# Optimization experiments

Hardware: AMD Instinct MI355X
Metric: run time of the kernel (lower is better)

## Reference

```python
import jax, jax.numpy as jnp
import numpy as np

GRID_SIZE = 5
SPLINE_ORDER = 3
NUM_BASIS = GRID_SIZE + SPLINE_ORDER  # 8
GRID = jnp.linspace(-1.0, 1.0, GRID_SIZE + 2 * SPLINE_ORDER + 1)  # [12]
EPS = 1e-6


def bspline_basis(x):
    """Iterative Cox-de Boor. x: [...]; returns [..., NUM_BASIS]."""
    xe = x[..., None]
    # order-0 indicator basis: [..., G-1]
    B = ((xe >= GRID[:-1]) & (xe < GRID[1:])).astype(x.dtype)
    for k in range(1, SPLINE_ORDER + 1):
        nb = B.shape[-1] - 1
        g_i = GRID[:nb]
        g_i1 = GRID[1:1 + nb]
        g_ik = GRID[k:k + nb]
        g_ik1 = GRID[k + 1:k + 1 + nb]
        dl = g_ik - g_i
        dr = g_ik1 - g_i1
        left = jnp.where(dl > EPS, (xe - g_i) / jnp.where(dl > EPS, dl, 1.0), 0.0) * B[..., :nb]
        right = jnp.where(dr > EPS, (g_ik1 - xe) / jnp.where(dr > EPS, dr, 1.0), 0.0) * B[..., 1:nb + 1]
        B = left + right
    return B[..., :NUM_BASIS]


def setup_inputs() -> dict:
    key = jax.random.key(0)
    k1, k2 = jax.random.split(key)
    x = jax.random.normal(k1, (8192, 512), dtype=jnp.float32)
    spline_coeffs = jax.random.normal(k2, (512, 512, NUM_BASIS), dtype=jnp.float32) * 0.1
    return {"x": x, "spline_coeffs": spline_coeffs}


def reference(x, spline_coeffs):
    xn = jnp.tanh(x)                       # [B, in]
    basis = bspline_basis(xn)              # [B, in, K]
    # output[b, o] = sum_{i,k} coeffs[o, i, k] * basis[b, i, k]
    return jnp.einsum('bik,oik->bo', basis, spline_coeffs)
```

## Files before the change

### kernel.cpp

```cpp
#include <hip/hip_runtime.h>
#include <hip/hip_bf16.h>
#include <stdint.h>


#define M_TOTAL 8192
#define N_DIM   512
#define K_DIM   4096
#define BM 128
#define BN 128
#define BK 64
#define NT_HALF 32
#define GRP_LDS 65536
#define BUF_HALF 32768

typedef __attribute__((ext_vector_type(8))) short short8;
typedef __attribute__((ext_vector_type(4))) float f32x4;
typedef __attribute__((ext_vector_type(16))) float f32x16;

typedef const __attribute__((address_space(1))) uint32_t ga_u32;
typedef __attribute__((address_space(3))) uint32_t ls_u32;

__device__ __forceinline__ void gload_lds16(const void* g, void* l) {
  __builtin_amdgcn_global_load_lds((ga_u32*)(uintptr_t)g,
                                   (ls_u32*)(uint32_t)(uintptr_t)l, 16, 0, 0);
}

__device__ __forceinline__ uint32_t f2bf(float f) {
  uint32_t u = __builtin_bit_cast(uint32_t, f);
  return (u + 0x7FFFu + ((u >> 16) & 1u)) >> 16;
}

__device__ __forceinline__ int swz(int r, int c) {
  return c ^ (r & 7) ^ (((r >> 4) & 1) << 2);
}

__device__ __forceinline__ void basis_slots(float xv, uint32_t o[4]) {
  xv = fminf(15.f, fmaxf(-15.f, xv));
  float e  = __expf(2.0f * xv);
  float t  = (e - 1.0f) * __builtin_amdgcn_rcpf(e + 1.0f);
  float uf = (t + 1.0f) * 5.5f;
  int   c  = (int)uf;  c = c > 10 ? 10 : c;
  float u  = uf - (float)c;
  float u2 = u * u, u3 = u2 * u, om = 1.0f - u;
  float w0 = om * om * om * (1.0f / 6.0f);
  float w1 = (3.0f * u3 - 6.0f * u2 + 4.0f) * (1.0f / 6.0f);
  float w2 = (-3.0f * u3 + 3.0f * u2 + 3.0f * u + 1.0f) * (1.0f / 6.0f);
  float w3 = u3 * (1.0f / 6.0f);
  uint32_t p01 = f2bf(w0) | (f2bf(w1) << 16);
  uint32_t p23 = f2bf(w2) | (f2bf(w3) << 16);
  uint64_t W = (uint64_t)p01 | ((uint64_t)p23 << 32);
  int d = c - 3;
  uint64_t lo = (d < 0) ? (W >> ((-d) * 16))
              : ((d < 4) ? (W << (d * 16)) : 0ull);
  uint64_t hi = (d <= 0) ? 0ull
              : ((d < 4) ? (W >> ((4 - d) * 16)) : (W << ((d - 4) * 16)));
  o[0] = (uint32_t)lo; o[1] = (uint32_t)(lo >> 32);
  o[2] = (uint32_t)hi; o[3] = (uint32_t)(hi >> 32);
}

__global__ __launch_bounds__(256) void basis_kernel(const float* __restrict__ x,
                                                    __hip_bfloat16* __restrict__ A,
                                                    int total) {
  int idx = blockIdx.x * 256 + threadIdx.x;
  if (idx >= total) return;
  uint32_t o[4];
  basis_slots(x[idx], o);
  reinterpret_cast<int4*>(A)[idx] = make_int4(o[0], o[1], o[2], o[3]);
}

__global__ __launch_bounds__(256) void cvt_kernel(const float* __restrict__ c,
                                                  __hip_bfloat16* __restrict__ Bt,
                                                  int total8) {
  int idx = blockIdx.x * 256 + threadIdx.x;
  if (idx >= total8) return;
  const float4* cp = reinterpret_cast<const float4*>(c) + (size_t)idx * 2;
  float4 a = cp[0], b = cp[1];
  union { unsigned short us[8]; int4 v; } pk;
  pk.us[0] = (unsigned short)f2bf(a.x); pk.us[1] = (unsigned short)f2bf(a.y);
  pk.us[2] = (unsigned short)f2bf(a.z); pk.us[3] = (unsigned short)f2bf(a.w);
  pk.us[4] = (unsigned short)f2bf(b.x); pk.us[5] = (unsigned short)f2bf(b.y);
  pk.us[6] = (unsigned short)f2bf(b.z); pk.us[7] = (unsigned short)f2bf(b.w);
  reinterpret_cast<int4*>(Bt)[idx] = pk.v;
}

__global__ __launch_bounds__(512) void gemm_kernel(
    const __hip_bfloat16* __restrict__ A,
    const __hip_bfloat16* __restrict__ Bt,
    float* __restrict__ C) {
  __shared__ char lds[2 * GRP_LDS];

  const int tid   = threadIdx.x;
  const int wid   = tid >> 6;
  const int lane  = tid & 63;
  const int l32   = lane & 31;
  const int lh    = lane >> 5;
  const int kgrp  = wid >> 2;
  const int w2    = wid & 3;
  const int waveM = w2 >> 1, waveN = w2 & 1;
  const int tg    = tid & 255;

  const int b  = blockIdx.x;
  const int q  = b >> 3;
  const int mt = (b & 7) * 8 + (q >> 2);
  const int nt = q & 3;
  const int m0 = mt * BM;
  const int n0 = nt * BN;

  char* grp = lds + kgrp * GRP_LDS;

  uint32_t aGlob[4], bGlob[4], sOff[4];
#pragma unroll
  for (int t = 0; t < 4; ++t) {
    int s = t * 256 + tg, row = s >> 3, p = s & 7, cc = swz(row, p);
    sOff[t]  = (uint32_t)s * 16u;
    aGlob[t] = (uint32_t)(m0 + row) * K_DIM + (uint32_t)cc * 8u
             + (uint32_t)kgrp * 2048u;
    bGlob[t] = (uint32_t)(n0 + row) * K_DIM + (uint32_t)cc * 8u
             + (uint32_t)kgrp * 2048u;
  }

  uint32_t aOff[4][2], bOff[4][2];
#pragma unroll
  for (int ks = 0; ks < 4; ++ks) {
    int c = ks * 2 + lh;
#pragma unroll
    for (int mi = 0; mi < 2; ++mi) {
      int row = waveM * 64 + mi * 32 + l32;
      aOff[ks][mi] = (uint32_t)(row * 8 + swz(row, c)) * 16u;
    }
#pragma unroll
    for (int ni = 0; ni < 2; ++ni) {
      int row = waveN * 64 + ni * 32 + l32;
      bOff[ks][ni] = 16384u + (uint32_t)(row * 8 + swz(row, c)) * 16u;
    }
  }

  f32x16 acc[2][2];
#pragma unroll
  for (int mi = 0; mi < 2; ++mi)
#pragma unroll
    for (int ni = 0; ni < 2; ++ni)
      acc[mi][ni] = (f32x16){0.f};

#pragma unroll
  for (int t = 0; t < 4; ++t) {
    gload_lds16(A + aGlob[t], grp + sOff[t]);
    gload_lds16(Bt + bGlob[t], grp + 16384 + sOff[t]);
  }

  for (int it = 0; it < NT_HALF; ++it) {
    const int cur = it & 1;
    char* bufc = grp + cur * BUF_HALF;
    __syncthreads();
    if (it + 1 < NT_HALF) {
      char* bufn = grp + (1 - cur) * BUF_HALF;
      uint32_t kt = (uint32_t)(it + 1) * BK;
#pragma unroll
      for (int t = 0; t < 4; ++t) {
        gload_lds16(A + aGlob[t] + kt, bufn + sOff[t]);
        gload_lds16(Bt + bGlob[t] + kt, bufn + 16384 + sOff[t]);
      }
    }
#pragma unroll
    for (int ks = 0; ks < 4; ++ks) {
      short8 af0 = *reinterpret_cast<const short8*>(bufc + aOff[ks][0]);
      short8 af1 = *reinterpret_cast<const short8*>(bufc + aOff[ks][1]);
      short8 bf0 = *reinterpret_cast<const short8*>(bufc + bOff[ks][0]);
      short8 bf1 = *reinterpret_cast<const short8*>(bufc + bOff[ks][1]);
      acc[0][0] = __builtin_amdgcn_mfma_f32_32x32x16_bf16(af0, bf0, acc[0][0], 0, 0, 0);
      acc[0][1] = __builtin_amdgcn_mfma_f32_32x32x16_bf16(af0, bf1, acc[0][1], 0, 0, 0);
      acc[1][0] = __builtin_amdgcn_mfma_f32_32x32x16_bf16(af1, bf0, acc[1][0], 0, 0, 0);
      acc[1][1] = __builtin_amdgcn_mfma_f32_32x32x16_bf16(af1, bf1, acc[1][1], 0, 0, 0);
    }
  }

  __syncthreads();
  if (kgrp == 1) {
#pragma unroll
    for (int mi = 0; mi < 2; ++mi)
#pragma unroll
      for (int ni = 0; ni < 2; ++ni) {
        int f = mi * 2 + ni;
#pragma unroll
        for (int j = 0; j < 4; ++j) {
          f32x4 v;
#pragma unroll
          for (int rr = 0; rr < 4; ++rr) v[rr] = acc[mi][ni][j * 4 + rr];
          *reinterpret_cast<f32x4*>(
              lds + w2 * 16384 + (f * 4 + j) * 1024 + lane * 16) = v;
        }
      }
  }
  __syncthreads();
  if (kgrp == 0) {
#pragma unroll
    for (int mi = 0; mi < 2; ++mi) {
#pragma unroll
      for (int ni = 0; ni < 2; ++ni) {
        int f = mi * 2 + ni;
        int col   = n0 + waveN * 64 + ni * 32 + l32;
        int rbase = m0 + waveM * 64 + mi * 32 + lh * 4;
#pragma unroll
        for (int j = 0; j < 4; ++j) {
          f32x4 oth = *reinterpret_cast<f32x4*>(
              lds + w2 * 16384 + (f * 4 + j) * 1024 + lane * 16);
#pragma unroll
          for (int rr = 0; rr < 4; ++rr) {
            int row = rbase + 8 * j + rr;
            C[(size_t)row * N_DIM + col] = acc[mi][ni][j * 4 + rr] + oth[rr];
          }
        }
      }
    }
  }
}

extern "C" void kernel_launch(void* const* d_in, const int* in_sizes, int n_in,
                              void* d_out, int out_size, void* d_ws, size_t ws_size,
                              hipStream_t stream) {
  const float* x    = (const float*)d_in[0];
  const float* coef = (const float*)d_in[1];
  float* out = (float*)d_out;

  __hip_bfloat16* Bt = (__hip_bfloat16*)d_ws;
  __hip_bfloat16* A  = (__hip_bfloat16*)((char*)d_ws + (size_t)4 * 1024 * 1024);

  const int total8 = N_DIM * K_DIM / 8;
  cvt_kernel<<<(total8 + 255) / 256, 256, 0, stream>>>(coef, Bt, total8);

  const int total = M_TOTAL * 512;
  basis_kernel<<<total / 256, 256, 0, stream>>>(x, A, total);

  gemm_kernel<<<(M_TOTAL / BM) * (N_DIM / BN), 512, 0, stream>>>(A, Bt, out);
}
```

Baseline: 121.9 us.

## Split K across four wave groups with larger per-wave tiles and tree reduction

Changes the GEMM from a 2-way to a 4-way in-block K split. Each pair of waves now owns the full 128-row M extent and half of N, which gives 4x2 MFMA tiles per wave and more register reuse of fragments. It uses a BK=32 pipeline stage with a new swizzle that packs two rows per 128B LDS line. Partial sums are combined through a two-level LDS tree reduction. The cost is more accumulator registers, extra reduction syncs, and smaller loads per stage.

```diff
diff --git a/kernel.cpp b/kernel.cpp
--- a/kernel.cpp
+++ b/kernel.cpp
@@ -8,10 +8,11 @@
 #define K_DIM   4096
 #define BM 128
 #define BN 128
-#define BK 64
-#define NT_HALF 32
-#define GRP_LDS 65536
-#define BUF_HALF 32768
+#define BK 32
+#define NGRP 4
+#define NT_G 32
+#define GRP_LDS 32768
+#define BUF_SZ 16384
 
 typedef __attribute__((ext_vector_type(8))) short short8;
 typedef __attribute__((ext_vector_type(4))) float f32x4;
@@ -30,8 +31,8 @@
   return (u + 0x7FFFu + ((u >> 16) & 1u)) >> 16;
 }
 
-__device__ __forceinline__ int swz(int r, int c) {
-  return c ^ (r & 7) ^ (((r >> 4) & 1) << 2);
+__device__ __forceinline__ int swz32(int r, int c) {
+  return (((r & 1) << 2) | c) ^ ((r >> 1) & 7) ^ (((r >> 4) & 1) << 2);
 }
 
 __device__ __forceinline__ void basis_slots(float xv, uint32_t o[4]) {
@@ -87,17 +88,16 @@
     const __hip_bfloat16* __restrict__ A,
     const __hip_bfloat16* __restrict__ Bt,
     float* __restrict__ C) {
-  __shared__ char lds[2 * GRP_LDS];
+  __shared__ char lds[NGRP * GRP_LDS];
 
   const int tid   = threadIdx.x;
   const int wid   = tid >> 6;
   const int lane  = tid & 63;
   const int l32   = lane & 31;
   const int lh    = lane >> 5;
-  const int kgrp  = wid >> 2;
-  const int w2    = wid & 3;
-  const int waveM = w2 >> 1, waveN = w2 & 1;
-  const int tg    = tid & 255;
+  const int kgrp  = wid >> 1;
+  const int waveN = wid & 1;
+  const int tg    = tid & 127;
 
   const int b  = blockIdx.x;
   const int q  = b >> 3;
@@ -111,33 +111,37 @@
   uint32_t aGlob[4], bGlob[4], sOff[4];
 #pragma unroll
   for (int t = 0; t < 4; ++t) {
-    int s = t * 256 + tg, row = s >> 3, p = s & 7, cc = swz(row, p);
+    int s  = t * 128 + tg;
+    int L  = s >> 3, sl = s & 7;
+    int u  = sl ^ (L & 7) ^ (((L >> 3) & 1) << 2);
+    int r  = 2 * L + (u >> 2);
+    int c  = u & 3;
     sOff[t]  = (uint32_t)s * 16u;
-    aGlob[t] = (uint32_t)(m0 + row) * K_DIM + (uint32_t)cc * 8u
-             + (uint32_t)kgrp * 2048u;
-    bGlob[t] = (uint32_t)(n0 + row) * K_DIM + (uint32_t)cc * 8u
-             + (uint32_t)kgrp * 2048u;
-  }
-
-  uint32_t aOff[4][2], bOff[4][2];
-#pragma unroll
-  for (int ks = 0; ks < 4; ++ks) {
+    aGlob[t] = (uint32_t)(m0 + r) * K_DIM + (uint32_t)c * 8u
+             + (uint32_t)kgrp * 1024u;
+    bGlob[t] = (uint32_t)(n0 + r) * K_DIM + (uint32_t)c * 8u
+             + (uint32_t)kgrp * 1024u;
+  }
+
+  uint32_t aOff[2][4], bOff[2][2];
+#pragma unroll
+  for (int ks = 0; ks < 2; ++ks) {
     int c = ks * 2 + lh;
 #pragma unroll
-    for (int mi = 0; mi < 2; ++mi) {
-      int row = waveM * 64 + mi * 32 + l32;
-      aOff[ks][mi] = (uint32_t)(row * 8 + swz(row, c)) * 16u;
+    for (int mi = 0; mi < 4; ++mi) {
+      int r = mi * 32 + l32;
+      aOff[ks][mi] = (uint32_t)((r >> 1) * 8 + swz32(r, c)) * 16u;
     }
 #pragma unroll
     for (int ni = 0; ni < 2; ++ni) {
-      int row = waveN * 64 + ni * 32 + l32;
-      bOff[ks][ni] = 16384u + (uint32_t)(row * 8 + swz(row, c)) * 16u;
-    }
-  }
-
-  f32x16 acc[2][2];
-#pragma unroll
-  for (int mi = 0; mi < 2; ++mi)
+      int r = waveN * 64 + ni * 32 + l32;
+      bOff[ks][ni] = 8192u + (uint32_t)((r >> 1) * 8 + swz32(r, c)) * 16u;
+    }
+  }
+
+  f32x16 acc[4][2];
+#pragma unroll
+  for (int mi = 0; mi < 4; ++mi)
 #pragma unroll
     for (int ni = 0; ni < 2; ++ni)
       acc[mi][ni] = (f32x16){0.f};
@@ -145,69 +149,103 @@
 #pragma unroll
   for (int t = 0; t < 4; ++t) {
     gload_lds16(A + aGlob[t], grp + sOff[t]);
-    gload_lds16(Bt + bGlob[t], grp + 16384 + sOff[t]);
-  }
-
-  for (int it = 0; it < NT_HALF; ++it) {
-    const int cur = it & 1;
-    char* bufc = grp + cur * BUF_HALF;
+    gload_lds16(Bt + bGlob[t], grp + 8192 + sOff[t]);
+  }
+
+  for (int it = 0; it < NT_G; ++it) {
+    char* bufc = grp + (it & 1) * BUF_SZ;
     __syncthreads();
-    if (it + 1 < NT_HALF) {
-      char* bufn = grp + (1 - cur) * BUF_HALF;
+    if (it + 1 < NT_G) {
+      char* bufn = grp + ((it + 1) & 1) * BUF_SZ;
       uint32_t kt = (uint32_t)(it + 1) * BK;
 #pragma unroll
       for (int t = 0; t < 4; ++t) {
         gload_lds16(A + aGlob[t] + kt, bufn + sOff[t]);
-        gload_lds16(Bt + bGlob[t] + kt, bufn + 16384 + sOff[t]);
+        gload_lds16(Bt + bGlob[t] + kt, bufn + 8192 + sOff[t]);
       }
     }
 #pragma unroll
-    for (int ks = 0; ks < 4; ++ks) {
-      short8 af0 = *reinterpret_cast<const short8*>(bufc + aOff[ks][0]);
-      short8 af1 = *reinterpret_cast<const short8*>(bufc + aOff[ks][1]);
-      short8 bf0 = *reinterpret_cast<const short8*>(bufc + bOff[ks][0]);
-      short8 bf1 = *reinterpret_cast<const short8*>(bufc + bOff[ks][1]);
-      acc[0][0] = __builtin_amdgcn_mfma_f32_32x32x16_bf16(af0, bf0, acc[0][0], 0, 0, 0);
-      acc[0][1] = __builtin_amdgcn_mfma_f32_32x32x16_bf16(af0, bf1, acc[0][1], 0, 0, 0);
-      acc[1][0] = __builtin_amdgcn_mfma_f32_32x32x16_bf16(af1, bf0, acc[1][0], 0, 0, 0);
-      acc[1][1] = __builtin_amdgcn_mfma_f32_32x32x16_bf16(af1, bf1, acc[1][1], 0, 0, 0);
-    }
-  }
-
-  __syncthreads();
-  if (kgrp == 1) {
-#pragma unroll
-    for (int mi = 0; mi < 2; ++mi)
-#pragma unroll
-      for (int ni = 0; ni < 2; ++ni) {
-        int f = mi * 2 + ni;
+    for (int ks = 0; ks < 2; ++ks) {
+      short8 af[4], bf[2];
+#pragma unroll
+      for (int mi = 0; mi < 4; ++mi)
+        af[mi] = *reinterpret_cast<const short8*>(bufc + aOff[ks][mi]);
+#pragma unroll
+      for (int ni = 0; ni < 2; ++ni)
+        bf[ni] = *reinterpret_cast<const short8*>(bufc + bOff[ks][ni]);
+#pragma unroll
+      for (int mi = 0; mi < 4; ++mi)
+#pragma unroll
+        for (int ni = 0; ni < 2; ++ni)
+          acc[mi][ni] = __builtin_amdgcn_mfma_f32_32x32x16_bf16(
+              af[mi], bf[ni], acc[mi][ni], 0, 0, 0);
+    }
+  }
+
+  __syncthreads();
+  if (kgrp & 1) {
+    char* dst = lds + (kgrp >> 1) * 65536 + waveN * 32768;
+#pragma unroll
+    for (int mi = 0; mi < 4; ++mi)
+#pragma unroll
+      for (int ni = 0; ni < 2; ++ni)
 #pragma unroll
         for (int j = 0; j < 4; ++j) {
           f32x4 v;
 #pragma unroll
           for (int rr = 0; rr < 4; ++rr) v[rr] = acc[mi][ni][j * 4 + rr];
           *reinterpret_cast<f32x4*>(
-              lds + w2 * 16384 + (f * 4 + j) * 1024 + lane * 16) = v;
-        }
-      }
+              dst + ((mi * 2 + ni) * 4 + j) * 1024 + lane * 16) = v;
+        }
+  }
+  __syncthreads();
+  if (!(kgrp & 1)) {
+    char* src = lds + (kgrp >> 1) * 65536 + waveN * 32768;
+#pragma unroll
+    for (int mi = 0; mi < 4; ++mi)
+#pragma unroll
+      for (int ni = 0; ni < 2; ++ni)
+#pragma unroll
+        for (int j = 0; j < 4; ++j) {
+          f32x4 o = *reinterpret_cast<f32x4*>(
+              src + ((mi * 2 + ni) * 4 + j) * 1024 + lane * 16);
+#pragma unroll
+          for (int rr = 0; rr < 4; ++rr) acc[mi][ni][j * 4 + rr] += o[rr];
+        }
+  }
+  __syncthreads();
+  if (kgrp == 2) {
+    char* dst = lds + waveN * 32768;
+#pragma unroll
+    for (int mi = 0; mi < 4; ++mi)
+#pragma unroll
+      for (int ni = 0; ni < 2; ++ni)
+#pragma unroll
+        for (int j = 0; j < 4; ++j) {
+          f32x4 v;
+#pragma unroll
+          for (int rr = 0; rr < 4; ++rr) v[rr] = acc[mi][ni][j * 4 + rr];
+          *reinterpret_cast<f32x4*>(
+              dst + ((mi * 2 + ni) * 4 + j) * 1024 + lane * 16) = v;
+        }
   }
   __syncthreads();
   if (kgrp == 0) {
-#pragma unroll
-    for (int mi = 0; mi < 2; ++mi) {
+    char* src = lds + waveN * 32768;
+#pragma unroll
+    for (int mi = 0; mi < 4; ++mi) {
 #pragma unroll
       for (int ni = 0; ni < 2; ++ni) {
-        int f = mi * 2 + ni;
         int col   = n0 + waveN * 64 + ni * 32 + l32;
-        int rbase = m0 + waveM * 64 + mi * 32 + lh * 4;
-#pragma unroll
-        for (int j = 0; j < 4; ++j) {
-          f32x4 oth = *reinterpret_cast<f32x4*>(
-              lds + w2 * 16384 + (f * 4 + j) * 1024 + lane * 16);
+        int rbase = m0 + mi * 32 + lh * 4;
+#pragma unroll
+        for (int j = 0; j < 4; ++j) {
+          f32x4 o = *reinterpret_cast<f32x4*>(
+              src + ((mi * 2 + ni) * 4 + j) * 1024 + lane * 16);
 #pragma unroll
           for (int rr = 0; rr < 4; ++rr) {
             int row = rbase + 8 * j + rr;
-            C[(size_t)row * N_DIM + col] = acc[mi][ni][j * 4 + rr] + oth[rr];
+            C[(size_t)row * N_DIM + col] = acc[mi][ni][j * 4 + rr] + o[rr];
           }
         }
       }
```

New measurement: 130.8 us. +7.3%, slower.
